# Optimization experiments

Measured on AMD Instinct MI355X. Metric: run time of the kernel, lower is better.

## Reference

```python
import jax, jax.numpy as jnp
import numpy as np
from jax import lax

N_NODES = 64; N_GROUPS = 16; GROUP_SIZE = 4
B = 256; L = 64; CNN_C = 32; GH = 128; DH = 128; OUT = 64
E1 = 262144; E2 = 32768
GROUP_NODES = jnp.arange(N_NODES).reshape(N_GROUPS, GROUP_SIZE)

PARAM_SHAPES = [
    ('conv_w3', (N_NODES, CNN_C, 3)), ('conv_b3', (N_NODES, CNN_C)),
    ('conv_w5', (N_NODES, CNN_C, 5)), ('conv_b5', (N_NODES, CNN_C)),
    ('conv_w7', (N_NODES, CNN_C, 7)), ('conv_b7', (N_NODES, CNN_C)),
    ('tconv_w3', (N_NODES, CNN_C, 3)), ('tconv_b3', (N_NODES, CNN_C)),
    ('tconv_w5', (N_NODES, CNN_C, 5)), ('tconv_b5', (N_NODES, CNN_C)),
    ('tconv_w7', (N_NODES, CNN_C, 7)), ('tconv_b7', (N_NODES, CNN_C)),
    ('ff_w', (N_NODES, 6 * CNN_C, GH)), ('ff_b', (N_NODES, GH)),
    ('lower_w', (GH, GH)), ('lower_b', (GH,)),
    ('upper_w', (GH, GH)), ('upper_b', (GH,)),
    ('agg_w', (N_GROUPS, GROUP_SIZE * GH, GH)), ('agg_b', (N_GROUPS, GH)),
    ('disc_w', (N_GROUPS, 2 * GH, DH)), ('disc_b', (N_GROUPS, DH)),
    ('fc_w', (N_GROUPS * DH, OUT)), ('fc_b', (OUT,)),
]


def setup_inputs() -> dict:
    key = jax.random.key(0)
    ks = jax.random.split(key, 6 + len(PARAM_SHAPES))
    d = {
        'x1': jax.random.normal(ks[0], (B * N_NODES, 4, L), jnp.float32),
        'x2': jax.random.normal(ks[1], (B * N_NODES, 4, L), jnp.float32),
        'edge_index1': jax.random.randint(ks[2], (2, E1), 0, B * N_NODES),
        'edge_index2': jax.random.randint(ks[3], (2, E1), 0, B * N_NODES),
        'group_edge_index1': jax.random.randint(ks[4], (2, E2), 0, B * N_GROUPS),
        'group_edge_index2': jax.random.randint(ks[5], (2, E2), 0, B * N_GROUPS),
    }
    for i, (name, shape) in enumerate(PARAM_SHAPES):
        d[name] = jax.random.normal(ks[6 + i], shape, jnp.float32) * 0.05
    return d


def _grouped_conv_max(x, w, b, pad):
    # x: [B, N, Lx] (one input channel per node), w: [N, C, k], b: [N, C]
    N, C, k = w.shape
    y = lax.conv_general_dilated(x, w.reshape(N * C, 1, k), (1,), [(pad, pad)],
                                 feature_group_count=N,
                                 dimension_numbers=('NCH', 'OIH', 'NCH'))
    y = y + b.reshape(1, N * C, 1)
    return y.max(axis=2).reshape(x.shape[0], N, C)  # max over time per channel


def _gcn(x, edge_index, W, bias):
    # PyG GCNConv: add self loops, symmetric D^-1/2 (A+I) D^-1/2 normalization
    n = x.shape[0]
    loops = jnp.arange(n)
    src = jnp.concatenate([edge_index[0], loops])
    dst = jnp.concatenate([edge_index[1], loops])
    deg = jax.ops.segment_sum(jnp.ones(src.shape[0], x.dtype), dst, n)
    dinv = jnp.where(deg > 0, lax.rsqrt(deg), 0.0)
    h = x @ W
    msg = h[src] * (dinv[src] * dinv[dst])[:, None]
    return jax.ops.segment_sum(msg, dst, n) + bias


def reference(x1, x2, edge_index1, edge_index2, group_edge_index1, group_edge_index2,
              conv_w3, conv_b3, conv_w5, conv_b5, conv_w7, conv_b7,
              tconv_w3, tconv_b3, tconv_w5, tconv_b5, tconv_w7, tconv_b7,
              ff_w, ff_b, lower_w, lower_b, upper_w, upper_b,
              agg_w, agg_b, disc_w, disc_b, fc_w, fc_b):
    def encode(x, ei, gei):
        xr = x.reshape(B, N_NODES, 4, L)  # row = b*N_NODES + n -> x[n::N] == xr[:, n]
        feats = jnp.concatenate([
            _grouped_conv_max(xr[:, :, 0, :], conv_w3, conv_b3, 1),
            _grouped_conv_max(xr[:, :, 0, :], conv_w5, conv_b5, 2),
            _grouped_conv_max(xr[:, :, 0, :], conv_w7, conv_b7, 3),
            _grouped_conv_max(xr[:, :, 1, :-2], tconv_w3, tconv_b3, 1),
            _grouped_conv_max(xr[:, :, 2, :-4], tconv_w5, tconv_b5, 2),
            _grouped_conv_max(xr[:, :, 3, :-6], tconv_w7, tconv_b7, 3),
        ], axis=2)  # [B, N, 6C]
        feats = jax.nn.relu(feats)
        h = jax.nn.relu(jnp.einsum('bnf,nfh->bnh', feats, ff_w) + ff_b)  # per-node Linear
        h = _gcn(h.reshape(B * N_NODES, GH), ei, lower_w, lower_b)
        hg = h.reshape(B, N_NODES, GH)[:, GROUP_NODES]  # [B, G, S, GH]
        hg = hg.reshape(B, N_GROUPS, GROUP_SIZE * GH)
        hg = jnp.einsum('bgf,gfh->bgh', hg, agg_w) + agg_b  # per-group aggregate Linear
        hg = _gcn(hg.reshape(B * N_GROUPS, GH), gei, upper_w, upper_b)
        return jax.nn.relu(hg).reshape(B, N_GROUPS, GH)

    h1 = encode(x1, edge_index1, group_edge_index1)
    h2 = encode(x2, edge_index2, group_edge_index2)
    d = jnp.concatenate([h1, h2], axis=2)  # [B, G, 2*GH]
    d = jax.nn.relu(jnp.einsum('bgf,gfd->bgd', d, disc_w) + disc_b)  # per-group disc fc
    return d.reshape(B, N_GROUPS * DH) @ fc_w + fc_b  # [B, OUT]
```

## Files before the change

kernel.cpp:

```cpp
#include <hip/hip_runtime.h>
#include <hip/hip_bf16.h>

namespace {

constexpr int Bn      = 256;
constexpr int NNODES  = 64;
constexpr int NGROUPS = 16;
constexpr int L       = 64;
constexpr int C       = 32;
constexpr int GH      = 128;
constexpr int E1      = 262144;
constexpr int E2      = 32768;
constexpr int NROWS   = Bn * NNODES;
constexpr int GROWS   = Bn * NGROUPS;

template<int K, int LX>
__device__ __forceinline__ float convmax(const float* __restrict__ xin,
                                         const float* __restrict__ wp)
{
    constexpr int PAD = (K - 1) / 2;
    float w[K];
    #pragma unroll
    for (int i = 0; i < K; ++i) w[i] = wp[i];
    float m = -3.0e38f;
    #pragma unroll
    for (int p = 0; p < LX; ++p) {
        float s = 0.f;
        #pragma unroll
        for (int i = 0; i < K; ++i) s = fmaf(w[i], xin[p - PAD + i], s);
        m = fmaxf(m, s);
    }
    return m;
}

__global__ __launch_bounds__(256) void k_conv_feats(
    const float* __restrict__ x1, const float* __restrict__ x2,
    const float* __restrict__ w3,  const float* __restrict__ b3,
    const float* __restrict__ w5,  const float* __restrict__ b5,
    const float* __restrict__ w7,  const float* __restrict__ b7,
    const float* __restrict__ tw3, const float* __restrict__ tb3,
    const float* __restrict__ tw5, const float* __restrict__ tb5,
    const float* __restrict__ tw7, const float* __restrict__ tb7,
    float* __restrict__ feats)
{
    __shared__ float xs[8 * 4 * 72];
    const int t = threadIdx.x;
    const int eb = blockIdx.x >> 11;
    const float* __restrict__ x = eb ? x2 : x1;
    const int row0 = (blockIdx.x & 2047) * 8;
    for (int idx = t; idx < 8 * 4 * 72; idx += 256) {
        const int r   = idx / 288;
        const int rem = idx - r * 288;
        const int c   = rem / 72;
        const int j   = rem - c * 72;
        const int l   = j - 3;
        float v = 0.f;
        if (l >= 0 && l < 64 - 2 * c)
            v = x[(size_t)(row0 + r) * 256 + c * 64 + l];
        xs[idx] = v;
    }
    __syncthreads();

    const int r  = t >> 5;
    const int ch = t & 31;
    const int rowl = row0 + r;
    const int n   = rowl & (NNODES - 1);
    const int wc  = n * C + ch;
    const float* xb0 = &xs[r * 288 + 0 * 72 + 3];
    const float* xb1 = &xs[r * 288 + 1 * 72 + 3];
    const float* xb2 = &xs[r * 288 + 2 * 72 + 3];
    const float* xb3 = &xs[r * 288 + 3 * 72 + 3];

    float* o = feats + (size_t)(eb * NROWS + rowl) * 192 + ch;
    o[0 * 32] = fmaxf(convmax<3, 64>(xb0, w3  + wc * 3) + b3[wc],  0.f);
    o[1 * 32] = fmaxf(convmax<5, 64>(xb0, w5  + wc * 5) + b5[wc],  0.f);
    o[2 * 32] = fmaxf(convmax<7, 64>(xb0, w7  + wc * 7) + b7[wc],  0.f);
    o[3 * 32] = fmaxf(convmax<3, 62>(xb1, tw3 + wc * 3) + tb3[wc], 0.f);
    o[4 * 32] = fmaxf(convmax<5, 60>(xb2, tw5 + wc * 5) + tb5[wc], 0.f);
    o[5 * 32] = fmaxf(convmax<7, 58>(xb3, tw7 + wc * 7) + tb7[wc], 0.f);
}

__global__ __launch_bounds__(256) void k_ff(
    const float* __restrict__ feats, const float* __restrict__ ffw,
    const float* __restrict__ ffb, float* __restrict__ h0)
{
    const int nb = blockIdx.x >> 6;
    const int n  = blockIdx.x & 63;
    const int t  = threadIdx.x;
    const int o  = t & 127;
    const int rh = t >> 7;
    __shared__ float fs[16 * 192];
    {
        float4* d4 = (float4*)fs;
        for (int i = t; i < 16 * 48; i += 256) {
            const int r = i / 48, c4 = i - r * 48;
            d4[i] = *(const float4*)(feats + ((size_t)(nb * 16 + r) * 64 + n) * 192 + c4 * 4);
        }
    }
    __syncthreads();
    const float* w = ffw + (size_t)n * 192 * 128 + o;
    float acc[8];
    #pragma unroll
    for (int r = 0; r < 8; ++r) acc[r] = 0.f;
    #pragma unroll 2
    for (int f = 0; f < 192; f += 4) {
        const float w0 = w[(f + 0) * 128];
        const float w1 = w[(f + 1) * 128];
        const float w2 = w[(f + 2) * 128];
        const float w3_ = w[(f + 3) * 128];
        #pragma unroll
        for (int r = 0; r < 8; ++r) {
            const float4 xv = *(const float4*)(fs + (rh * 8 + r) * 192 + f);
            acc[r] = fmaf(xv.x, w0, acc[r]);
            acc[r] = fmaf(xv.y, w1, acc[r]);
            acc[r] = fmaf(xv.z, w2, acc[r]);
            acc[r] = fmaf(xv.w, w3_, acc[r]);
        }
    }
    const float bias = ffb[n * 128 + o];
    #pragma unroll
    for (int r = 0; r < 8; ++r) {
        const int row = nb * 16 + rh * 8 + r;
        h0[((size_t)row * 64 + n) * 128 + o] = fmaxf(acc[r] + bias, 0.f);
    }
}

__global__ __launch_bounds__(256) void k_gemm128(
    const float* __restrict__ X, const float* __restrict__ W,
    float* __restrict__ Y)
{
    const int r0 = blockIdx.x * 16;
    const int t  = threadIdx.x;
    const int o  = t & 127;
    const int rh = t >> 7;
    __shared__ float xs[16 * 128];
    {
        float4* d4 = (float4*)xs;
        const float4* s4 = (const float4*)(X + (size_t)r0 * 128);
        for (int i = t; i < 512; i += 256) d4[i] = s4[i];
    }
    __syncthreads();
    const float* w = W + o;
    float acc[8];
    #pragma unroll
    for (int r = 0; r < 8; ++r) acc[r] = 0.f;
    #pragma unroll 2
    for (int f = 0; f < 128; f += 4) {
        const float w0 = w[(f + 0) * 128];
        const float w1 = w[(f + 1) * 128];
        const float w2 = w[(f + 2) * 128];
        const float w3_ = w[(f + 3) * 128];
        #pragma unroll
        for (int r = 0; r < 8; ++r) {
            const float4 xv = *(const float4*)(xs + (rh * 8 + r) * 128 + f);
            acc[r] = fmaf(xv.x, w0, acc[r]);
            acc[r] = fmaf(xv.y, w1, acc[r]);
            acc[r] = fmaf(xv.z, w2, acc[r]);
            acc[r] = fmaf(xv.w, w3_, acc[r]);
        }
    }
    #pragma unroll
    for (int r = 0; r < 8; ++r)
        Y[(size_t)(r0 + rh * 8 + r) * 128 + o] = acc[r];
}

__global__ void k_zero_i(int* __restrict__ p, int n) {
    const int i = blockIdx.x * blockDim.x + threadIdx.x;
    if (i < n) p[i] = 0;
}
__global__ void k_hist2(const int* __restrict__ eia, const int* __restrict__ eib,
                        int* __restrict__ cnt, int E, int n)
{
    const int gid = blockIdx.x * blockDim.x + threadIdx.x;
    const int eb = gid >= E;
    const int le = gid - (eb ? E : 0);
    if (le >= E) return;
    const int* ei = eb ? eib : eia;
    atomicAdd(&cnt[(eb ? n : 0) + ei[E + le]], 1);
}
__global__ __launch_bounds__(256) void k_scan_bsum(
    const int* __restrict__ cnt, int* __restrict__ bsum)
{
    const int t = threadIdx.x;
    const int4 v = ((const int4*)cnt)[blockIdx.x * 256 + t];
    int s = v.x + v.y + v.z + v.w;
    #pragma unroll
    for (int off = 32; off > 0; off >>= 1) s += __shfl_down(s, off);
    __shared__ int wsum[4];
    if ((t & 63) == 0) wsum[t >> 6] = s;
    __syncthreads();
    if (t == 0) bsum[blockIdx.x] = wsum[0] + wsum[1] + wsum[2] + wsum[3];
}
__global__ __launch_bounds__(256) void k_scan_final(
    const int* __restrict__ cnt, const int* __restrict__ bsum, int nb,
    int* __restrict__ offs, int* __restrict__ cur, float* __restrict__ dinv, int n)
{
    const int blk = blockIdx.x, t = threadIdx.x;
    int base = 0;
    for (int i = 0; i < blk; ++i) base += bsum[i];
    const int4 v = ((const int4*)cnt)[blk * 256 + t];
    const int s = v.x + v.y + v.z + v.w;
    int sc = s;
    #pragma unroll
    for (int off = 1; off < 64; off <<= 1) {
        const int u = __shfl_up(sc, off);
        if ((t & 63) >= off) sc += u;
    }
    __shared__ int wsum[4];
    if ((t & 63) == 63) wsum[t >> 6] = sc;
    __syncthreads();
    int wbase = 0;
    for (int wv = 0; wv < (t >> 6); ++wv) wbase += wsum[wv];
    int o0 = base + wbase + sc - s;
    const int gi = blk * 1024 + t * 4;
    offs[gi + 0] = o0; cur[gi + 0] = o0; dinv[gi + 0] = rsqrtf(1.f + (float)v.x); o0 += v.x;
    offs[gi + 1] = o0; cur[gi + 1] = o0; dinv[gi + 1] = rsqrtf(1.f + (float)v.y); o0 += v.y;
    offs[gi + 2] = o0; cur[gi + 2] = o0; dinv[gi + 2] = rsqrtf(1.f + (float)v.z); o0 += v.z;
    offs[gi + 3] = o0; cur[gi + 3] = o0; dinv[gi + 3] = rsqrtf(1.f + (float)v.w); o0 += v.w;
    if (blk == nb - 1 && t == 255) offs[n] = o0;
}
__global__ void k_fill2(const int* __restrict__ eia, const int* __restrict__ eib,
                        int* __restrict__ cur, int* __restrict__ esrc, int E, int n)
{
    const int gid = blockIdx.x * blockDim.x + threadIdx.x;
    const int eb = gid >= E;
    const int le = gid - (eb ? E : 0);
    if (le >= E) return;
    const int* ei = eb ? eib : eia;
    const int s = ei[le];
    const int d = ei[E + le];
    const int pos = atomicAdd(&cur[(eb ? n : 0) + d], 1);
    esrc[pos] = s;
}

__global__ __launch_bounds__(128) void k_gcn_gather(
    const int* __restrict__ offs, const int* __restrict__ esrc,
    const float* __restrict__ hw, const float* __restrict__ dinv,
    const float* __restrict__ bias, float* __restrict__ out, int n)
{
    const int d = blockIdx.x;
    const int t = threadIdx.x;
    const int sbase = (d >= n) ? n : 0;
    const int e0 = offs[d], e1 = offs[d + 1];
    const float dd = dinv[d];
    float a0 = hw[(size_t)d * 128 + t] * dd;
    float a1 = 0.f, a2 = 0.f, a3 = 0.f;
    int j = e0;
    for (; j + 3 < e1; j += 4) {
        const int s0 = sbase + esrc[j],     s1 = sbase + esrc[j + 1];
        const int s2 = sbase + esrc[j + 2], s3 = sbase + esrc[j + 3];
        a0 = fmaf(hw[(size_t)s0 * 128 + t], dinv[s0], a0);
        a1 = fmaf(hw[(size_t)s1 * 128 + t], dinv[s1], a1);
        a2 = fmaf(hw[(size_t)s2 * 128 + t], dinv[s2], a2);
        a3 = fmaf(hw[(size_t)s3 * 128 + t], dinv[s3], a3);
    }
    for (; j < e1; ++j) {
        const int s = sbase + esrc[j];
        a0 = fmaf(hw[(size_t)s * 128 + t], dinv[s], a0);
    }
    const float acc = (a0 + a1) + (a2 + a3);
    out[(size_t)d * 128 + t] = fmaf(acc, dd, bias[t]);
}

__global__ __launch_bounds__(256) void k_agg(
    const float* __restrict__ h, const float* __restrict__ aggw,
    const float* __restrict__ aggb, float* __restrict__ hg)
{
    const int bt = blockIdx.x >> 4;
    const int g  = blockIdx.x & 15;
    const int t  = threadIdx.x;
    const int o  = t & 127;
    const int kk = t >> 7;
    __shared__ float fs[4 * 512];
    __shared__ float red[2][4][128];
    {
        const int b0 = bt * 4;
        float4* dst = (float4*)fs;
        for (int i = t; i < 4 * 128; i += 256) {
            const int r = i >> 7;
            const int q = i & 127;
            dst[i] = *(const float4*)(h + ((size_t)(b0 + r) * 64 + g * 4) * 128 + q * 4);
        }
    }
    __syncthreads();
    const float* w = aggw + (size_t)g * 512 * 128 + (size_t)kk * 256 * 128 + o;
    float a0 = 0.f, a1 = 0.f, a2 = 0.f, a3 = 0.f;
    const float* x0 = fs + 0 * 512 + kk * 256;
    const float* x1 = fs + 1 * 512 + kk * 256;
    const float* x2 = fs + 2 * 512 + kk * 256;
    const float* x3 = fs + 3 * 512 + kk * 256;
    #pragma unroll 8
    for (int f = 0; f < 256; ++f) {
        const float wv = w[f * 128];
        a0 = fmaf(x0[f], wv, a0);
        a1 = fmaf(x1[f], wv, a1);
        a2 = fmaf(x2[f], wv, a2);
        a3 = fmaf(x3[f], wv, a3);
    }
    red[kk][0][o] = a0; red[kk][1][o] = a1; red[kk][2][o] = a2; red[kk][3][o] = a3;
    __syncthreads();
    if (t < 128) {
        const float bias = aggb[g * 128 + t];
        #pragma unroll
        for (int r = 0; r < 4; ++r) {
            const int b = bt * 4 + r;
            hg[((size_t)b * 16 + g) * 128 + t] = red[0][r][t] + red[1][r][t] + bias;
        }
    }
}

__global__ __launch_bounds__(256) void k_disc(
    const float* __restrict__ h1, const float* __restrict__ h2,
    const float* __restrict__ dw, const float* __restrict__ db,
    float* __restrict__ dd)
{
    const int bt = blockIdx.x >> 4;
    const int g  = blockIdx.x & 15;
    const int t  = threadIdx.x;
    const int o  = t & 127;
    const int kk = t >> 7;
    __shared__ float fs[4 * 256];
    __shared__ float red[2][4][128];
    {
        const int half = t >> 7;
        #pragma unroll
        for (int r = 0; r < 4; ++r) {
            const int rowi = ((bt * 4 + r) * 16 + g);
            const float* src = half ? h2 : h1;
            fs[r * 256 + half * 128 + o] = fmaxf(src[(size_t)rowi * 128 + o], 0.f);
        }
    }
    __syncthreads();
    const float* w = dw + (size_t)g * 256 * 128 + (size_t)kk * 128 * 128 + o;
    float a0 = 0.f, a1 = 0.f, a2 = 0.f, a3 = 0.f;
    const float* x0 = fs + 0 * 256 + kk * 128;
    const float* x1 = fs + 1 * 256 + kk * 128;
    const float* x2 = fs + 2 * 256 + kk * 128;
    const float* x3 = fs + 3 * 256 + kk * 128;
    #pragma unroll 8
    for (int f = 0; f < 128; ++f) {
        const float wv = w[f * 128];
        a0 = fmaf(x0[f], wv, a0);
        a1 = fmaf(x1[f], wv, a1);
        a2 = fmaf(x2[f], wv, a2);
        a3 = fmaf(x3[f], wv, a3);
    }
    red[kk][0][o] = a0; red[kk][1][o] = a1; red[kk][2][o] = a2; red[kk][3][o] = a3;
    __syncthreads();
    if (t < 128) {
        const float bias = db[g * 128 + t];
        #pragma unroll
        for (int r = 0; r < 4; ++r) {
            const int b = bt * 4 + r;
            dd[(size_t)b * 2048 + g * 128 + t] =
                fmaxf(red[0][r][t] + red[1][r][t] + bias, 0.f);
        }
    }
}

__global__ __launch_bounds__(256) void k_fc(
    const float* __restrict__ dd, const float* __restrict__ fcw,
    const float* __restrict__ fcb, float* __restrict__ out)
{
    const int b = blockIdx.x;
    const int t = threadIdx.x;
    const int o = t & 63;
    const int k = t >> 6;
    __shared__ float ds[2048];
    __shared__ float red[4][64];
    for (int i = t; i < 2048; i += 256) ds[i] = dd[(size_t)b * 2048 + i];
    __syncthreads();
    const float* w  = fcw + (k * 512) * 64 + o;
    const float* xr = ds + k * 512;
    float a0 = 0.f, a1 = 0.f, a2 = 0.f, a3 = 0.f;
    #pragma unroll 4
    for (int f = 0; f < 512; f += 4) {
        a0 = fmaf(xr[f + 0], w[(f + 0) * 64], a0);
        a1 = fmaf(xr[f + 1], w[(f + 1) * 64], a1);
        a2 = fmaf(xr[f + 2], w[(f + 2) * 64], a2);
        a3 = fmaf(xr[f + 3], w[(f + 3) * 64], a3);
    }
    red[k][o] = (a0 + a1) + (a2 + a3);
    __syncthreads();
    if (t < 64)
        out[(size_t)b * 64 + t] = ((red[0][t] + red[1][t]) + (red[2][t] + red[3][t])) + fcb[t];
}

}

extern "C" void kernel_launch(void* const* d_in, const int* in_sizes, int n_in,
                              void* d_out, int out_size, void* d_ws, size_t ws_size,
                              hipStream_t stream)
{
    const float* x1 = (const float*)d_in[0];
    const float* x2 = (const float*)d_in[1];
    const int* ei0  = (const int*)d_in[2];
    const int* ei1  = (const int*)d_in[3];
    const int* gei0 = (const int*)d_in[4];
    const int* gei1 = (const int*)d_in[5];
    const float* conv_w3 = (const float*)d_in[6];
    const float* conv_b3 = (const float*)d_in[7];
    const float* conv_w5 = (const float*)d_in[8];
    const float* conv_b5 = (const float*)d_in[9];
    const float* conv_w7 = (const float*)d_in[10];
    const float* conv_b7 = (const float*)d_in[11];
    const float* tconv_w3 = (const float*)d_in[12];
    const float* tconv_b3 = (const float*)d_in[13];
    const float* tconv_w5 = (const float*)d_in[14];
    const float* tconv_b5 = (const float*)d_in[15];
    const float* tconv_w7 = (const float*)d_in[16];
    const float* tconv_b7 = (const float*)d_in[17];
    const float* ff_w    = (const float*)d_in[18];
    const float* ff_b    = (const float*)d_in[19];
    const float* lower_w = (const float*)d_in[20];
    const float* lower_b = (const float*)d_in[21];
    const float* upper_w = (const float*)d_in[22];
    const float* upper_b = (const float*)d_in[23];
    const float* agg_w   = (const float*)d_in[24];
    const float* agg_b   = (const float*)d_in[25];
    const float* disc_w  = (const float*)d_in[26];
    const float* disc_b  = (const float*)d_in[27];
    const float* fc_w    = (const float*)d_in[28];
    const float* fc_b    = (const float*)d_in[29];

    float* ws = (float*)d_ws;
    float* f_feats = ws;
    float* f_h0    = ws + 6291456;
    float* f_hw    = ws + 10485760;
    float* f_gout  = ws + 14680064;
    float* f_hg    = ws + 18874368;
    float* f_hgw   = ws + 19922944;
    float* f_henc  = ws + 20971520;
    float* f_dd    = ws + 22020096;
    float* f_dinv1 = ws + 22544384;
    float* f_dinv2 = ws + 22577152;
    int* ip    = (int*)(ws + 22585344);
    int* cnt1  = ip;
    int* cnt2  = cnt1 + 2 * NROWS;
    int* offs1 = cnt2 + 2 * GROWS;
    int* cur1  = offs1 + 2 * NROWS + 1;
    int* esrc1 = cur1 + 2 * NROWS;
    int* offs2 = esrc1 + 2 * E1;
    int* cur2  = offs2 + 2 * GROWS + 1;
    int* esrc2 = cur2 + 2 * GROWS;
    int* bsum1 = esrc2 + 2 * E2;
    int* bsum2 = bsum1 + 32;

    k_zero_i<<<(2 * NROWS) / 256, 256, 0, stream>>>(cnt1, 2 * NROWS);
    k_hist2<<<(2 * E1) / 256, 256, 0, stream>>>(ei0, ei1, cnt1, E1, NROWS);
    k_scan_bsum<<<32, 256, 0, stream>>>(cnt1, bsum1);
    k_scan_final<<<32, 256, 0, stream>>>(cnt1, bsum1, 32, offs1, cur1, f_dinv1, 2 * NROWS);
    k_fill2<<<(2 * E1) / 256, 256, 0, stream>>>(ei0, ei1, cur1, esrc1, E1, NROWS);
    k_zero_i<<<(2 * GROWS) / 256, 256, 0, stream>>>(cnt2, 2 * GROWS);
    k_hist2<<<(2 * E2) / 256, 256, 0, stream>>>(gei0, gei1, cnt2, E2, GROWS);
    k_scan_bsum<<<8, 256, 0, stream>>>(cnt2, bsum2);
    k_scan_final<<<8, 256, 0, stream>>>(cnt2, bsum2, 8, offs2, cur2, f_dinv2, 2 * GROWS);
    k_fill2<<<(2 * E2) / 256, 256, 0, stream>>>(gei0, gei1, cur2, esrc2, E2, GROWS);

    k_conv_feats<<<2 * NROWS / 8, 256, 0, stream>>>(x1, x2,
        conv_w3, conv_b3, conv_w5, conv_b5, conv_w7, conv_b7,
        tconv_w3, tconv_b3, tconv_w5, tconv_b5, tconv_w7, tconv_b7, f_feats);
    k_ff<<<2048, 256, 0, stream>>>(f_feats, ff_w, ff_b, f_h0);
    k_gemm128<<<2 * NROWS / 16, 256, 0, stream>>>(f_h0, lower_w, f_hw);
    k_gcn_gather<<<2 * NROWS, 128, 0, stream>>>(offs1, esrc1, f_hw, f_dinv1,
                                                lower_b, f_gout, NROWS);
    k_agg<<<2 * (Bn / 4) * 16, 256, 0, stream>>>(f_gout, agg_w, agg_b, f_hg);
    k_gemm128<<<2 * GROWS / 16, 256, 0, stream>>>(f_hg, upper_w, f_hgw);
    k_gcn_gather<<<2 * GROWS, 128, 0, stream>>>(offs2, esrc2, f_hgw, f_dinv2,
                                                upper_b, f_henc, GROWS);

    k_disc<<<(Bn / 4) * 16, 256, 0, stream>>>(f_henc, f_henc + (size_t)GROWS * 128,
                                              disc_w, disc_b, f_dd);
    k_fc<<<Bn, 256, 0, stream>>>(f_dd, fc_w, fc_b, (float*)d_out);
}
```

Before: 294.2 us.

## Fuse ff with lower GEMM, register-block conv, merge graph preprocessing kernels

Fuses the per-node feed-forward layer with the lower GCN weight GEMM, so the intermediate h0 stays in shared memory and is never written to or read back from global memory. Merges the two edge-index histogram, scan and fill pipelines into single launches to cut kernel-launch count. Restructures the conv kernel so each thread computes two channels with float4-loaded register windows, processing 16 rows per block. This raises register pressure in the conv and reduces grid size, and relies on the cnt2 buffer sitting directly after cnt1 for the combined zeroing.

Measured after the change: 283.2 us. 3.7% less time.

```diff
diff --git a/kernel.cpp b/kernel.cpp
--- a/kernel.cpp
+++ b/kernel.cpp
@@ -15,22 +15,44 @@
 constexpr int GROWS   = Bn * NGROUPS;
 
 template<int K, int LX>
-__device__ __forceinline__ float convmax(const float* __restrict__ xin,
-                                         const float* __restrict__ wp)
+__device__ __forceinline__ void convmax2(const float* __restrict__ xin_al,
+                                         const float* __restrict__ wpa,
+                                         const float* __restrict__ wpb,
+                                         float& ma, float& mb)
 {
     constexpr int PAD = (K - 1) / 2;
-    float w[K];
+    constexpr int OFF = 3 - PAD;
+    float wa[K], wb[K];
     #pragma unroll
-    for (int i = 0; i < K; ++i) w[i] = wp[i];
-    float m = -3.0e38f;
+    for (int i = 0; i < K; ++i) { wa[i] = wpa[i]; wb[i] = wpb[i]; }
+    ma = -3.0e38f; mb = -3.0e38f;
     #pragma unroll
-    for (int p = 0; p < LX; ++p) {
-        float s = 0.f;
-        #pragma unroll
-        for (int i = 0; i < K; ++i) s = fmaf(w[i], xin[p - PAD + i], s);
-        m = fmaxf(m, s);
-    }
-    return m;
+    for (int p0 = 0; p0 < LX; p0 += 16) {
+        float xw[24];
+        #pragma unroll
+        for (int q = 0; q < 6; ++q) {
+            const float4 v = *(const float4*)(xin_al + p0 + q * 4);
+            xw[q * 4 + 0] = v.x; xw[q * 4 + 1] = v.y;
+            xw[q * 4 + 2] = v.z; xw[q * 4 + 3] = v.w;
+        }
+        #pragma unroll
+        for (int p = 0; p < 16; p += 2) {
+            if (p0 + p + 1 < LX) {
+                float sa0 = 0.f, sb0 = 0.f, sa1 = 0.f, sb1 = 0.f;
+                #pragma unroll
+                for (int i = 0; i < K; ++i) {
+                    const float xv0 = xw[p + OFF + i];
+                    const float xv1 = xw[p + 1 + OFF + i];
+                    sa0 = fmaf(wa[i], xv0, sa0);
+                    sb0 = fmaf(wb[i], xv0, sb0);
+                    sa1 = fmaf(wa[i], xv1, sa1);
+                    sb1 = fmaf(wb[i], xv1, sb1);
+                }
+                ma = fmaxf(fmaxf(sa0, sa1), ma);
+                mb = fmaxf(fmaxf(sb0, sb1), mb);
+            }
+        }
+    }
 }
 
 __global__ __launch_bounds__(256) void k_conv_feats(
@@ -43,12 +65,12 @@
     const float* __restrict__ tw7, const float* __restrict__ tb7,
     float* __restrict__ feats)
 {
-    __shared__ float xs[8 * 4 * 72];
+    __shared__ float xs[16 * 4 * 72];
     const int t = threadIdx.x;
-    const int eb = blockIdx.x >> 11;
+    const int eb = blockIdx.x >> 10;
     const float* __restrict__ x = eb ? x2 : x1;
-    const int row0 = (blockIdx.x & 2047) * 8;
-    for (int idx = t; idx < 8 * 4 * 72; idx += 256) {
+    const int row0 = (blockIdx.x & 1023) * 16;
+    for (int idx = t; idx < 16 * 4 * 72; idx += 256) {
         const int r   = idx / 288;
         const int rem = idx - r * 288;
         const int c   = rem / 72;
@@ -61,28 +83,39 @@
     }
     __syncthreads();
 
-    const int r  = t >> 5;
-    const int ch = t & 31;
-    const int rowl = row0 + r;
-    const int n   = rowl & (NNODES - 1);
-    const int wc  = n * C + ch;
-    const float* xb0 = &xs[r * 288 + 0 * 72 + 3];
-    const float* xb1 = &xs[r * 288 + 1 * 72 + 3];
-    const float* xb2 = &xs[r * 288 + 2 * 72 + 3];
-    const float* xb3 = &xs[r * 288 + 3 * 72 + 3];
-
-    float* o = feats + (size_t)(eb * NROWS + rowl) * 192 + ch;
-    o[0 * 32] = fmaxf(convmax<3, 64>(xb0, w3  + wc * 3) + b3[wc],  0.f);
-    o[1 * 32] = fmaxf(convmax<5, 64>(xb0, w5  + wc * 5) + b5[wc],  0.f);
-    o[2 * 32] = fmaxf(convmax<7, 64>(xb0, w7  + wc * 7) + b7[wc],  0.f);
-    o[3 * 32] = fmaxf(convmax<3, 62>(xb1, tw3 + wc * 3) + tb3[wc], 0.f);
-    o[4 * 32] = fmaxf(convmax<5, 60>(xb2, tw5 + wc * 5) + tb5[wc], 0.f);
-    o[5 * 32] = fmaxf(convmax<7, 58>(xb3, tw7 + wc * 7) + tb7[wc], 0.f);
-}
-
-__global__ __launch_bounds__(256) void k_ff(
+    const int rr  = t >> 4;
+    const int cp  = t & 15;
+    const int ch0 = cp * 2;
+    const int row = row0 + rr;
+    const int n   = row & (NNODES - 1);
+    const int wc0 = n * C + ch0;
+    const int wc1 = wc0 + 1;
+    const float* xb0 = &xs[rr * 288 + 0 * 72];
+    const float* xb1 = &xs[rr * 288 + 1 * 72];
+    const float* xb2 = &xs[rr * 288 + 2 * 72];
+    const float* xb3 = &xs[rr * 288 + 3 * 72];
+
+    float ma, mb;
+    float* o = feats + (size_t)(eb * NROWS + row) * 192 + ch0;
+
+    convmax2<3, 64>(xb0, w3 + wc0 * 3, w3 + wc1 * 3, ma, mb);
+    *(float2*)(o + 0 * 32) = make_float2(fmaxf(ma + b3[wc0], 0.f), fmaxf(mb + b3[wc1], 0.f));
+    convmax2<5, 64>(xb0, w5 + wc0 * 5, w5 + wc1 * 5, ma, mb);
+    *(float2*)(o + 1 * 32) = make_float2(fmaxf(ma + b5[wc0], 0.f), fmaxf(mb + b5[wc1], 0.f));
+    convmax2<7, 64>(xb0, w7 + wc0 * 7, w7 + wc1 * 7, ma, mb);
+    *(float2*)(o + 2 * 32) = make_float2(fmaxf(ma + b7[wc0], 0.f), fmaxf(mb + b7[wc1], 0.f));
+    convmax2<3, 62>(xb1, tw3 + wc0 * 3, tw3 + wc1 * 3, ma, mb);
+    *(float2*)(o + 3 * 32) = make_float2(fmaxf(ma + tb3[wc0], 0.f), fmaxf(mb + tb3[wc1], 0.f));
+    convmax2<5, 60>(xb2, tw5 + wc0 * 5, tw5 + wc1 * 5, ma, mb);
+    *(float2*)(o + 4 * 32) = make_float2(fmaxf(ma + tb5[wc0], 0.f), fmaxf(mb + tb5[wc1], 0.f));
+    convmax2<7, 58>(xb3, tw7 + wc0 * 7, tw7 + wc1 * 7, ma, mb);
+    *(float2*)(o + 5 * 32) = make_float2(fmaxf(ma + tb7[wc0], 0.f), fmaxf(mb + tb7[wc1], 0.f));
+}
+
+__global__ __launch_bounds__(256) void k_ff_lower(
     const float* __restrict__ feats, const float* __restrict__ ffw,
-    const float* __restrict__ ffb, float* __restrict__ h0)
+    const float* __restrict__ ffb, const float* __restrict__ lw,
+    float* __restrict__ hw)
 {
     const int nb = blockIdx.x >> 6;
     const int n  = blockIdx.x & 63;
@@ -90,6 +123,7 @@
     const int o  = t & 127;
     const int rh = t >> 7;
     __shared__ float fs[16 * 192];
+    __shared__ float h0s[16 * 128];
     {
         float4* d4 = (float4*)fs;
         for (int i = t; i < 16 * 48; i += 256) {
@@ -98,30 +132,57 @@
         }
     }
     __syncthreads();
-    const float* w = ffw + (size_t)n * 192 * 128 + o;
-    float acc[8];
-    #pragma unroll
-    for (int r = 0; r < 8; ++r) acc[r] = 0.f;
-    #pragma unroll 2
-    for (int f = 0; f < 192; f += 4) {
-        const float w0 = w[(f + 0) * 128];
-        const float w1 = w[(f + 1) * 128];
-        const float w2 = w[(f + 2) * 128];
-        const float w3_ = w[(f + 3) * 128];
+    {
+        const float* w = ffw + (size_t)n * 192 * 128 + o;
+        float acc[8];
+        #pragma unroll
+        for (int r = 0; r < 8; ++r) acc[r] = 0.f;
+        #pragma unroll 2
+        for (int f = 0; f < 192; f += 4) {
+            const float w0 = w[(f + 0) * 128];
+            const float w1 = w[(f + 1) * 128];
+            const float w2 = w[(f + 2) * 128];
+            const float w3_ = w[(f + 3) * 128];
+            #pragma unroll
+            for (int r = 0; r < 8; ++r) {
+                const float4 xv = *(const float4*)(fs + (rh * 8 + r) * 192 + f);
+                acc[r] = fmaf(xv.x, w0, acc[r]);
+                acc[r] = fmaf(xv.y, w1, acc[r]);
+                acc[r] = fmaf(xv.z, w2, acc[r]);
+                acc[r] = fmaf(xv.w, w3_, acc[r]);
+            }
+        }
+        const float bias = ffb[n * 128 + o];
+        #pragma unroll
+        for (int r = 0; r < 8; ++r)
+            h0s[(rh * 8 + r) * 128 + o] = fmaxf(acc[r] + bias, 0.f);
+    }
+    __syncthreads();
+    {
+        const float* w = lw + o;
+        float acc[8];
+        #pragma unroll
+        for (int r = 0; r < 8; ++r) acc[r] = 0.f;
+        #pragma unroll 2
+        for (int f = 0; f < 128; f += 4) {
+            const float w0 = w[(f + 0) * 128];
+            const float w1 = w[(f + 1) * 128];
+            const float w2 = w[(f + 2) * 128];
+            const float w3_ = w[(f + 3) * 128];
+            #pragma unroll
+            for (int r = 0; r < 8; ++r) {
+                const float4 xv = *(const float4*)(h0s + (rh * 8 + r) * 128 + f);
+                acc[r] = fmaf(xv.x, w0, acc[r]);
+                acc[r] = fmaf(xv.y, w1, acc[r]);
+                acc[r] = fmaf(xv.z, w2, acc[r]);
+                acc[r] = fmaf(xv.w, w3_, acc[r]);
+            }
+        }
         #pragma unroll
         for (int r = 0; r < 8; ++r) {
-            const float4 xv = *(const float4*)(fs + (rh * 8 + r) * 192 + f);
-            acc[r] = fmaf(xv.x, w0, acc[r]);
-            acc[r] = fmaf(xv.y, w1, acc[r]);
-            acc[r] = fmaf(xv.z, w2, acc[r]);
-            acc[r] = fmaf(xv.w, w3_, acc[r]);
-        }
-    }
-    const float bias = ffb[n * 128 + o];
-    #pragma unroll
-    for (int r = 0; r < 8; ++r) {
-        const int row = nb * 16 + rh * 8 + r;
-        h0[((size_t)row * 64 + n) * 128 + o] = fmaxf(acc[r] + bias, 0.f);
+            const int row = nb * 16 + rh * 8 + r;
+            hw[((size_t)row * 64 + n) * 128 + o] = acc[r];
+        }
     }
 }
 
@@ -168,37 +229,57 @@
     const int i = blockIdx.x * blockDim.x + threadIdx.x;
     if (i < n) p[i] = 0;
 }
-__global__ void k_hist2(const int* __restrict__ eia, const int* __restrict__ eib,
-                        int* __restrict__ cnt, int E, int n)
+__global__ void k_hist_all(const int* __restrict__ ei0, const int* __restrict__ ei1,
+                           const int* __restrict__ gei0, const int* __restrict__ gei1,
+                           int* __restrict__ cnt1, int* __restrict__ cnt2)
 {
     const int gid = blockIdx.x * blockDim.x + threadIdx.x;
-    const int eb = gid >= E;
-    const int le = gid - (eb ? E : 0);
-    if (le >= E) return;
-    const int* ei = eb ? eib : eia;
-    atomicAdd(&cnt[(eb ? n : 0) + ei[E + le]], 1);
-}
-__global__ __launch_bounds__(256) void k_scan_bsum(
-    const int* __restrict__ cnt, int* __restrict__ bsum)
-{
-    const int t = threadIdx.x;
-    const int4 v = ((const int4*)cnt)[blockIdx.x * 256 + t];
+    if (gid < 2 * E1) {
+        const int eb = gid >= E1;
+        const int le = gid - (eb ? E1 : 0);
+        const int* ei = eb ? ei1 : ei0;
+        atomicAdd(&cnt1[(eb ? NROWS : 0) + ei[E1 + le]], 1);
+    } else {
+        const int g2 = gid - 2 * E1;
+        const int eb = g2 >= E2;
+        const int le = g2 - (eb ? E2 : 0);
+        const int* ei = eb ? gei1 : gei0;
+        atomicAdd(&cnt2[(eb ? GROWS : 0) + ei[E2 + le]], 1);
+    }
+}
+__global__ __launch_bounds__(256) void k_scan_bsum_all(
+    const int* __restrict__ cnt1, const int* __restrict__ cnt2,
+    int* __restrict__ bsum1, int* __restrict__ bsum2)
+{
+    const int blk = blockIdx.x, t = threadIdx.x;
+    const int* cnt; int* bsum; int lblk;
+    if (blk < 32) { cnt = cnt1; bsum = bsum1; lblk = blk; }
+    else          { cnt = cnt2; bsum = bsum2; lblk = blk - 32; }
+    const int4 v = ((const int4*)cnt)[lblk * 256 + t];
     int s = v.x + v.y + v.z + v.w;
     #pragma unroll
     for (int off = 32; off > 0; off >>= 1) s += __shfl_down(s, off);
     __shared__ int wsum[4];
     if ((t & 63) == 0) wsum[t >> 6] = s;
     __syncthreads();
-    if (t == 0) bsum[blockIdx.x] = wsum[0] + wsum[1] + wsum[2] + wsum[3];
-}
-__global__ __launch_bounds__(256) void k_scan_final(
-    const int* __restrict__ cnt, const int* __restrict__ bsum, int nb,
-    int* __restrict__ offs, int* __restrict__ cur, float* __restrict__ dinv, int n)
+    if (t == 0) bsum[lblk] = wsum[0] + wsum[1] + wsum[2] + wsum[3];
+}
+__global__ __launch_bounds__(256) void k_scan_final_all(
+    const int* __restrict__ cnt1, const int* __restrict__ bsum1,
+    int* __restrict__ offs1, int* __restrict__ cur1, float* __restrict__ dinv1,
+    const int* __restrict__ cnt2, const int* __restrict__ bsum2,
+    int* __restrict__ offs2, int* __restrict__ cur2, float* __restrict__ dinv2)
 {
     const int blk = blockIdx.x, t = threadIdx.x;
+    const int* cnt; const int* bsum; int* offs; int* cur; float* dinv;
+    int n, nb, lblk;
+    if (blk < 32) { cnt = cnt1; bsum = bsum1; offs = offs1; cur = cur1; dinv = dinv1;
+                    n = 2 * NROWS; nb = 32; lblk = blk; }
+    else          { cnt = cnt2; bsum = bsum2; offs = offs2; cur = cur2; dinv = dinv2;
+                    n = 2 * GROWS; nb = 8; lblk = blk - 32; }
     int base = 0;
-    for (int i = 0; i < blk; ++i) base += bsum[i];
-    const int4 v = ((const int4*)cnt)[blk * 256 + t];
+    for (int i = 0; i < lblk; ++i) base += bsum[i];
+    const int4 v = ((const int4*)cnt)[lblk * 256 + t];
     const int s = v.x + v.y + v.z + v.w;
     int sc = s;
     #pragma unroll
@@ -212,25 +293,37 @@
     int wbase = 0;
     for (int wv = 0; wv < (t >> 6); ++wv) wbase += wsum[wv];
     int o0 = base + wbase + sc - s;
-    const int gi = blk * 1024 + t * 4;
+    const int gi = lblk * 1024 + t * 4;
     offs[gi + 0] = o0; cur[gi + 0] = o0; dinv[gi + 0] = rsqrtf(1.f + (float)v.x); o0 += v.x;
     offs[gi + 1] = o0; cur[gi + 1] = o0; dinv[gi + 1] = rsqrtf(1.f + (float)v.y); o0 += v.y;
     offs[gi + 2] = o0; cur[gi + 2] = o0; dinv[gi + 2] = rsqrtf(1.f + (float)v.z); o0 += v.z;
     offs[gi + 3] = o0; cur[gi + 3] = o0; dinv[gi + 3] = rsqrtf(1.f + (float)v.w); o0 += v.w;
-    if (blk == nb - 1 && t == 255) offs[n] = o0;
-}
-__global__ void k_fill2(const int* __restrict__ eia, const int* __restrict__ eib,
-                        int* __restrict__ cur, int* __restrict__ esrc, int E, int n)
+    if (lblk == nb - 1 && t == 255) offs[n] = o0;
+}
+__global__ void k_fill_all(const int* __restrict__ ei0, const int* __restrict__ ei1,
+                           const int* __restrict__ gei0, const int* __restrict__ gei1,
+                           int* __restrict__ cur1, int* __restrict__ esrc1,
+                           int* __restrict__ cur2, int* __restrict__ esrc2)
 {
     const int gid = blockIdx.x * blockDim.x + threadIdx.x;
-    const int eb = gid >= E;
-    const int le = gid - (eb ? E : 0);
-    if (le >= E) return;
-    const int* ei = eb ? eib : eia;
-    const int s = ei[le];
-    const int d = ei[E + le];
-    const int pos = atomicAdd(&cur[(eb ? n : 0) + d], 1);
-    esrc[pos] = s;
+    if (gid < 2 * E1) {
+        const int eb = gid >= E1;
+        const int le = gid - (eb ? E1 : 0);
+        const int* ei = eb ? ei1 : ei0;
+        const int s = ei[le];
+        const int d = ei[E1 + le];
+        const int pos = atomicAdd(&cur1[(eb ? NROWS : 0) + d], 1);
+        esrc1[pos] = s;
+    } else {
+        const int g2 = gid - 2 * E1;
+        const int eb = g2 >= E2;
+        const int le = g2 - (eb ? E2 : 0);
+        const int* ei = eb ? gei1 : gei0;
+        const int s = ei[le];
+        const int d = ei[E2 + le];
+        const int pos = atomicAdd(&cur2[(eb ? GROWS : 0) + d], 1);
+        esrc2[pos] = s;
+    }
 }
 
 __global__ __launch_bounds__(128) void k_gcn_gather(
@@ -425,7 +518,6 @@
 
     float* ws = (float*)d_ws;
     float* f_feats = ws;
-    float* f_h0    = ws + 6291456;
     float* f_hw    = ws + 10485760;
     float* f_gout  = ws + 14680064;
     float* f_hg    = ws + 18874368;
@@ -446,22 +538,18 @@
     int* bsum1 = esrc2 + 2 * E2;
     int* bsum2 = bsum1 + 32;
 
-    k_zero_i<<<(2 * NROWS) / 256, 256, 0, stream>>>(cnt1, 2 * NROWS);
-    k_hist2<<<(2 * E1) / 256, 256, 0, stream>>>(ei0, ei1, cnt1, E1, NROWS);
-    k_scan_bsum<<<32, 256, 0, stream>>>(cnt1, bsum1);
-    k_scan_final<<<32, 256, 0, stream>>>(cnt1, bsum1, 32, offs1, cur1, f_dinv1, 2 * NROWS);
-    k_fill2<<<(2 * E1) / 256, 256, 0, stream>>>(ei0, ei1, cur1, esrc1, E1, NROWS);
-    k_zero_i<<<(2 * GROWS) / 256, 256, 0, stream>>>(cnt2, 2 * GROWS);
-    k_hist2<<<(2 * E2) / 256, 256, 0, stream>>>(gei0, gei1, cnt2, E2, GROWS);
-    k_scan_bsum<<<8, 256, 0, stream>>>(cnt2, bsum2);
-    k_scan_final<<<8, 256, 0, stream>>>(cnt2, bsum2, 8, offs2, cur2, f_dinv2, 2 * GROWS);
-    k_fill2<<<(2 * E2) / 256, 256, 0, stream>>>(gei0, gei1, cur2, esrc2, E2, GROWS);
-
-    k_conv_feats<<<2 * NROWS / 8, 256, 0, stream>>>(x1, x2,
+    k_zero_i<<<(2 * NROWS + 2 * GROWS) / 256, 256, 0, stream>>>(cnt1, 2 * NROWS + 2 * GROWS);
+    k_hist_all<<<(2 * E1 + 2 * E2) / 256, 256, 0, stream>>>(ei0, ei1, gei0, gei1, cnt1, cnt2);
+    k_scan_bsum_all<<<40, 256, 0, stream>>>(cnt1, cnt2, bsum1, bsum2);
+    k_scan_final_all<<<40, 256, 0, stream>>>(cnt1, bsum1, offs1, cur1, f_dinv1,
+                                             cnt2, bsum2, offs2, cur2, f_dinv2);
+    k_fill_all<<<(2 * E1 + 2 * E2) / 256, 256, 0, stream>>>(ei0, ei1, gei0, gei1,
+                                                            cur1, esrc1, cur2, esrc2);
+
+    k_conv_feats<<<2 * NROWS / 16, 256, 0, stream>>>(x1, x2,
         conv_w3, conv_b3, conv_w5, conv_b5, conv_w7, conv_b7,
         tconv_w3, tconv_b3, tconv_w5, tconv_b5, tconv_w7, tconv_b7, f_feats);
-    k_ff<<<2048, 256, 0, stream>>>(f_feats, ff_w, ff_b, f_h0);
-    k_gemm128<<<2 * NROWS / 16, 256, 0, stream>>>(f_h0, lower_w, f_hw);
+    k_ff_lower<<<2048, 256, 0, stream>>>(f_feats, ff_w, ff_b, lower_w, f_hw);
     k_gcn_gather<<<2 * NROWS, 128, 0, stream>>>(offs1, esrc1, f_hw, f_dinv1,
                                                 lower_b, f_gout, NROWS);
     k_agg<<<2 * (Bn / 4) * 16, 256, 0, stream>>>(f_gout, agg_w, agg_b, f_hg);
```
